# Kernel optimization log

Hardware: AMD Instinct MI355X
Metric: run time of the kernel (lower is better)

Reference implementation:

```python
import jax, jax.numpy as jnp
import numpy as np


def setup_inputs() -> dict:
    key = jax.random.key(0)
    k1, k2 = jax.random.split(key)
    B, N, M, D = 8, 8192, 8192, 3
    x = jax.random.normal(k1, (B, N, D), dtype=jnp.float32)
    y = jax.random.normal(k2, (B, M, D), dtype=jnp.float32)
    return {"x": x, "y": y}


def reference(x, y):
    # dist[b, i, j] = |x_bi|^2 + |y_bj|^2 - 2 * <x_bi, y_bj>
    # (same math as the torch code's rx.transpose(2,1) + ry - 2*xy, but
    #  computed with row-norm vectors instead of full NxN / MxM bmms)
    xx = jnp.sum(x * x, axis=-1)                      # [B, N]
    yy = jnp.sum(y * y, axis=-1)                      # [B, M]
    xy = jnp.einsum('bnd,bmd->bnm', x, y)             # [B, N, M]
    dist = xx[:, :, None] + yy[:, None, :] - 2.0 * xy # [B, N, M]
    dist1 = jnp.min(dist, axis=1)  # min over x points -> per-y nearest  [B, M]
    dist2 = jnp.min(dist, axis=2)  # min over y points -> per-x nearest  [B, N]
    return jnp.mean(dist1) + jnp.mean(dist2)
```

## Files before the change

### kernel.cpp

```cpp
#include <hip/hip_runtime.h>


#define B_ 8
#define N_ 8192
#define PTS (B_ * N_)
#define TPB 512

typedef short bf16x8 __attribute__((ext_vector_type(8)));
typedef float f32x16 __attribute__((ext_vector_type(16)));

__device__ __forceinline__ unsigned b16(float f) {
  unsigned u = __float_as_uint(f);
  return (u + 0x7FFFu + ((u >> 16) & 1u)) >> 16;
}
__device__ __forceinline__ float bf(unsigned h) { return __uint_as_float(h << 16); }

__device__ __forceinline__ void build_chunk(const float* __restrict__ cb,
                                            uint4* __restrict__ dst, int t) {
  const unsigned one = 0x3F80u;
#pragma unroll
  for (int q = 0; q < 2; ++q) {
    int p = t + q * TPB;
    float c0 = cb[3 * p], c1 = cb[3 * p + 1], c2 = cb[3 * p + 2];
    float nc = fmaf(c0, c0, fmaf(c1, c1, c2 * c2));
    unsigned yh0 = b16(c0), yh1 = b16(c1), yh2 = b16(c2);
    unsigned yl0 = b16(c0 - bf(yh0)), yl1 = b16(c1 - bf(yh1)), yl2 = b16(c2 - bf(yh2));
    unsigned nh = b16(nc), nl = b16(nc - bf(nh));
    int tt = p >> 5, mm = p & 31;
    dst[tt * 64 + mm]      = make_uint4(yh0 | (yh1 << 16), yh2 | (yl0 << 16),
                                        yl1 | (yl2 << 16), yh0 | (yh1 << 16));
    dst[tt * 64 + 32 + mm] = make_uint4(yh2 | (one << 16), one | (nh << 16),
                                        nl, 0u);
  }
}

__global__ __launch_bounds__(TPB, 2) void chamfer_main_k(
    const float* __restrict__ x, const float* __restrict__ y,
    float* __restrict__ gpart) {
  __shared__ uint4 ldsFrag[2][32 * 64];

  const unsigned one = 0x3F80u;
  int t = threadIdx.x, lane = t & 63, w = t >> 6;
  int b = blockIdx.x;
  int g = b >> 1;
  int hf = b & 1;
  int dir = g >> 6;
  int gg = g & 63;
  int batch = gg >> 3;
  int seg = gg & 7;
  const float* __restrict__ own  = dir ? y : x;
  const float* __restrict__ cand = dir ? x : y;

  int m = lane & 31;
  int rowBase = batch * N_ + seg * 1024 + w * 128;
  bf16x8 A[4];
#pragma unroll
  for (int a = 0; a < 4; ++a) {
    const float* po = own + 3 * (rowBase + a * 32 + m);
    float v0 = po[0], v1 = po[1], v2 = po[2];
    float nv = fmaf(v0, v0, fmaf(v1, v1, v2 * v2));
    float a0 = -2.0f * v0, a1 = -2.0f * v1, a2 = -2.0f * v2;
    unsigned ah0 = b16(a0), ah1 = b16(a1), ah2 = b16(a2);
    unsigned al0 = b16(a0 - bf(ah0)), al1 = b16(a1 - bf(ah1)), al2 = b16(a2 - bf(ah2));
    unsigned nh = b16(nv), nl = b16(nv - bf(nh));
    uint4 h0 = make_uint4(ah0 | (ah1 << 16), ah2 | (ah0 << 16),
                          ah1 | (ah2 << 16), al0 | (al1 << 16));
    uint4 h1 = make_uint4(al2 | (nh << 16), nl | (one << 16), one, 0u);
    uint4 afr;
    afr.x = (lane < 32) ? h0.x : h1.x;
    afr.y = (lane < 32) ? h0.y : h1.y;
    afr.z = (lane < 32) ? h0.z : h1.z;
    afr.w = (lane < 32) ? h0.w : h1.w;
    A[a] = __builtin_bit_cast(bf16x8, afr);
  }

  f32x16 z = {0.f,0.f,0.f,0.f,0.f,0.f,0.f,0.f,0.f,0.f,0.f,0.f,0.f,0.f,0.f,0.f};
  f32x16 rm[4];
#pragma unroll
  for (int a = 0; a < 4; ++a)
#pragma unroll
    for (int r = 0; r < 16; ++r) rm[a][r] = 1e30f;

  const float* cbb = cand + (batch * N_ + hf * 4096) * 3;
  build_chunk(cbb, ldsFrag[0], t);
  __syncthreads();

  for (int ch = 0; ch < 4; ++ch) {
    const uint4* cur = ldsFrag[ch & 1];
    if (ch < 3)
      build_chunk(cbb + (ch + 1) * 1024 * 3, ldsFrag[(ch + 1) & 1], t);

    for (int i = 0; i < 16; ++i) {
      bf16x8 B0 = __builtin_bit_cast(bf16x8, cur[(2 * i) * 64 + lane]);
      bf16x8 B1 = __builtin_bit_cast(bf16x8, cur[(2 * i + 1) * 64 + lane]);
#pragma unroll
      for (int a = 0; a < 4; ++a) {
        f32x16 acc0 = __builtin_amdgcn_mfma_f32_32x32x16_bf16(A[a], B0, z, 0, 0, 0);
        f32x16 acc1 = __builtin_amdgcn_mfma_f32_32x32x16_bf16(A[a], B1, z, 0, 0, 0);
#pragma unroll
        for (int r = 0; r < 16; ++r)
          rm[a][r] = fminf(fminf(rm[a][r], acc0[r]), acc1[r]);
      }
    }
    __syncthreads();
  }

#pragma unroll
  for (int a = 0; a < 4; ++a)
#pragma unroll
    for (int msk = 1; msk <= 16; msk <<= 1)
#pragma unroll
      for (int r = 0; r < 16; ++r)
        rm[a][r] = fminf(rm[a][r], __shfl_xor(rm[a][r], msk, 64));

  float* gp = gpart + b * 1024;
  if ((lane & 31) == 0) {
    int h = lane >> 5;
#pragma unroll
    for (int a = 0; a < 4; ++a)
#pragma unroll
      for (int r = 0; r < 16; ++r)
        gp[w * 128 + a * 32 + (r & 3) + 8 * (r >> 2) + 4 * h] = rm[a][r];
  }
}

__global__ __launch_bounds__(256) void chamfer_final_k(
    const float* __restrict__ gpart, float* __restrict__ out) {
  int i = blockIdx.x * 256 + threadIdx.x;
  float s = 0.0f;
#pragma unroll
  for (int e = 0; e < 4; ++e) {
    int rowid = 4 * i + e;
    int g = rowid >> 10, r = rowid & 1023;
    s += fminf(gpart[(2 * g) * 1024 + r], gpart[(2 * g + 1) * 1024 + r]);
  }
  for (int off = 32; off > 0; off >>= 1) s += __shfl_down(s, off, 64);
  __shared__ float red[4];
  int lane = threadIdx.x & 63, wv = threadIdx.x >> 6;
  if (lane == 0) red[wv] = s;
  __syncthreads();
  if (threadIdx.x == 0) {
    float tt = (red[0] + red[1]) + (red[2] + red[3]);
    atomicAdd(out, tt * (1.0f / (float)PTS));
  }
}

extern "C" void kernel_launch(void* const* d_in, const int* in_sizes, int n_in,
                              void* d_out, int out_size, void* d_ws, size_t ws_size,
                              hipStream_t stream) {
  const float* x = (const float*)d_in[0];
  const float* y = (const float*)d_in[1];
  float* out = (float*)d_out;
  float* gpart = (float*)d_ws;

  hipMemsetAsync(out, 0, sizeof(float), stream);
  chamfer_main_k<<<256, TPB, 0, stream>>>(x, y, gpart);
  chamfer_final_k<<<128, 256, 0, stream>>>(gpart, out);
}
```

Baseline: 95.11 us.

## Halve rows per wave and double block count for higher occupancy

After: 94.07 us. About the same (-1.1%).

```diff
diff --git a/kernel.cpp b/kernel.cpp
--- a/kernel.cpp
+++ b/kernel.cpp
@@ -34,7 +34,7 @@
   }
 }
 
-__global__ __launch_bounds__(TPB, 2) void chamfer_main_k(
+__global__ __launch_bounds__(TPB, 4) void chamfer_main_k(
     const float* __restrict__ x, const float* __restrict__ y,
     float* __restrict__ gpart) {
   __shared__ uint4 ldsFrag[2][32 * 64];
@@ -44,18 +44,18 @@
   int b = blockIdx.x;
   int g = b >> 1;
   int hf = b & 1;
-  int dir = g >> 6;
-  int gg = g & 63;
-  int batch = gg >> 3;
-  int seg = gg & 7;
+  int dir = g >> 7;
+  int gg = g & 127;
+  int batch = gg >> 4;
+  int seg = gg & 15;
   const float* __restrict__ own  = dir ? y : x;
   const float* __restrict__ cand = dir ? x : y;
 
   int m = lane & 31;
-  int rowBase = batch * N_ + seg * 1024 + w * 128;
-  bf16x8 A[4];
+  int rowBase = batch * N_ + seg * 512 + w * 64;
+  bf16x8 A0, A1;
 #pragma unroll
-  for (int a = 0; a < 4; ++a) {
+  for (int a = 0; a < 2; ++a) {
     const float* po = own + 3 * (rowBase + a * 32 + m);
     float v0 = po[0], v1 = po[1], v2 = po[2];
     float nv = fmaf(v0, v0, fmaf(v1, v1, v2 * v2));
@@ -71,15 +71,14 @@
     afr.y = (lane < 32) ? h0.y : h1.y;
     afr.z = (lane < 32) ? h0.z : h1.z;
     afr.w = (lane < 32) ? h0.w : h1.w;
-    A[a] = __builtin_bit_cast(bf16x8, afr);
+    if (a == 0) A0 = __builtin_bit_cast(bf16x8, afr);
+    else        A1 = __builtin_bit_cast(bf16x8, afr);
   }
 
   f32x16 z = {0.f,0.f,0.f,0.f,0.f,0.f,0.f,0.f,0.f,0.f,0.f,0.f,0.f,0.f,0.f,0.f};
-  f32x16 rm[4];
+  f32x16 rm0, rm1;
 #pragma unroll
-  for (int a = 0; a < 4; ++a)
-#pragma unroll
-    for (int r = 0; r < 16; ++r) rm[a][r] = 1e30f;
+  for (int r = 0; r < 16; ++r) { rm0[r] = 1e30f; rm1[r] = 1e30f; }
 
   const float* cbb = cand + (batch * N_ + hf * 4096) * 3;
   build_chunk(cbb, ldsFrag[0], t);
@@ -90,37 +89,40 @@
     if (ch < 3)
       build_chunk(cbb + (ch + 1) * 1024 * 3, ldsFrag[(ch + 1) & 1], t);
 
+#pragma unroll 2
     for (int i = 0; i < 16; ++i) {
       bf16x8 B0 = __builtin_bit_cast(bf16x8, cur[(2 * i) * 64 + lane]);
       bf16x8 B1 = __builtin_bit_cast(bf16x8, cur[(2 * i + 1) * 64 + lane]);
+      f32x16 acc0 = __builtin_amdgcn_mfma_f32_32x32x16_bf16(A0, B0, z, 0, 0, 0);
+      f32x16 acc1 = __builtin_amdgcn_mfma_f32_32x32x16_bf16(A1, B0, z, 0, 0, 0);
+      f32x16 acc2 = __builtin_amdgcn_mfma_f32_32x32x16_bf16(A0, B1, z, 0, 0, 0);
+      f32x16 acc3 = __builtin_amdgcn_mfma_f32_32x32x16_bf16(A1, B1, z, 0, 0, 0);
 #pragma unroll
-      for (int a = 0; a < 4; ++a) {
-        f32x16 acc0 = __builtin_amdgcn_mfma_f32_32x32x16_bf16(A[a], B0, z, 0, 0, 0);
-        f32x16 acc1 = __builtin_amdgcn_mfma_f32_32x32x16_bf16(A[a], B1, z, 0, 0, 0);
-#pragma unroll
-        for (int r = 0; r < 16; ++r)
-          rm[a][r] = fminf(fminf(rm[a][r], acc0[r]), acc1[r]);
+      for (int r = 0; r < 16; ++r) {
+        rm0[r] = fminf(fminf(rm0[r], acc0[r]), acc2[r]);
+        rm1[r] = fminf(fminf(rm1[r], acc1[r]), acc3[r]);
       }
     }
     __syncthreads();
   }
 
 #pragma unroll
-  for (int a = 0; a < 4; ++a)
+  for (int msk = 1; msk <= 16; msk <<= 1)
 #pragma unroll
-    for (int msk = 1; msk <= 16; msk <<= 1)
-#pragma unroll
-      for (int r = 0; r < 16; ++r)
-        rm[a][r] = fminf(rm[a][r], __shfl_xor(rm[a][r], msk, 64));
+    for (int r = 0; r < 16; ++r) {
+      rm0[r] = fminf(rm0[r], __shfl_xor(rm0[r], msk, 64));
+      rm1[r] = fminf(rm1[r], __shfl_xor(rm1[r], msk, 64));
+    }
 
-  float* gp = gpart + b * 1024;
+  float* gp = gpart + b * 512;
   if ((lane & 31) == 0) {
     int h = lane >> 5;
 #pragma unroll
-    for (int a = 0; a < 4; ++a)
-#pragma unroll
-      for (int r = 0; r < 16; ++r)
-        gp[w * 128 + a * 32 + (r & 3) + 8 * (r >> 2) + 4 * h] = rm[a][r];
+    for (int r = 0; r < 16; ++r) {
+      int rr = (r & 3) + 8 * (r >> 2) + 4 * h;
+      gp[w * 64 + rr] = rm0[r];
+      gp[w * 64 + 32 + rr] = rm1[r];
+    }
   }
 }
 
@@ -131,8 +133,8 @@
 #pragma unroll
   for (int e = 0; e < 4; ++e) {
     int rowid = 4 * i + e;
-    int g = rowid >> 10, r = rowid & 1023;
-    s += fminf(gpart[(2 * g) * 1024 + r], gpart[(2 * g + 1) * 1024 + r]);
+    int g = rowid >> 9, r = rowid & 511;
+    s += fminf(gpart[(2 * g) * 512 + r], gpart[(2 * g + 1) * 512 + r]);
   }
   for (int off = 32; off > 0; off >>= 1) s += __shfl_down(s, off, 64);
   __shared__ float red[4];
@@ -154,6 +156,6 @@
   float* gpart = (float*)d_ws;
 
   hipMemsetAsync(out, 0, sizeof(float), stream);
-  chamfer_main_k<<<256, TPB, 0, stream>>>(x, y, gpart);
+  chamfer_main_k<<<512, TPB, 0, stream>>>(x, y, gpart);
   chamfer_final_k<<<128, 256, 0, stream>>>(gpart, out);
 }
```
